# Optimization experiments

Hardware: AMD Instinct MI355X
Metric: run time of the kernel (lower is better)

The kernel has to match this reference:

```python
import jax, jax.numpy as jnp
import numpy as np

N = 50000        # num_nodes
E = 800000       # num_edges
D_IN = 128
D_OUT = 128
BN_EPS = 1e-5    # torch BatchNorm1d default


def setup_inputs() -> dict:
    key = jax.random.key(0)
    ks = jax.random.split(key, 6)
    x = jax.random.normal(ks[0], (N, D_IN), dtype=jnp.float32)
    edge_index = jax.random.randint(ks[1], (2, E), 0, N, dtype=jnp.int64)
    eps = jnp.zeros((1,), dtype=jnp.float32)  # nn.Parameter(torch.tensor([0.0]))
    lim1 = 1.0 / np.sqrt(D_IN)
    lim2 = 1.0 / np.sqrt(D_OUT)
    W1 = jax.random.uniform(ks[2], (D_OUT, D_IN), jnp.float32, -lim1, lim1)
    b1 = jax.random.uniform(ks[3], (D_OUT,), jnp.float32, -lim1, lim1)
    W2 = jax.random.uniform(ks[4], (D_OUT, D_OUT), jnp.float32, -lim2, lim2)
    b2 = jax.random.uniform(ks[5], (D_OUT,), jnp.float32, -lim2, lim2)
    gamma1 = jnp.ones((D_OUT,), jnp.float32)
    beta1 = jnp.zeros((D_OUT,), jnp.float32)
    gamma2 = jnp.ones((D_OUT,), jnp.float32)
    beta2 = jnp.zeros((D_OUT,), jnp.float32)
    return {"x": x, "edge_index": edge_index, "eps": eps,
            "W1": W1, "b1": b1, "gamma1": gamma1, "beta1": beta1,
            "W2": W2, "b2": b2, "gamma2": gamma2, "beta2": beta2}


def _batch_norm(h, gamma, beta):
    # training-mode BatchNorm1d: biased batch variance, eps=1e-5
    mu = h.mean(axis=0)
    var = h.var(axis=0)
    return gamma * (h - mu) * jax.lax.rsqrt(var + BN_EPS) + beta


def reference(x, edge_index, eps, W1, b1, gamma1, beta1, W2, b2, gamma2, beta2):
    row, col = edge_index[0], edge_index[1]
    # agg[v] = sum_{(v,u) in edges} x[u]   (gather + scatter-add)
    agg = jax.ops.segment_sum(x[col], row, num_segments=N)  # [N, D_IN]
    out = (1.0 + eps) * x + agg                              # [N, D_IN]
    h = jax.nn.relu(_batch_norm(out @ W1.T + b1, gamma1, beta1))
    h = jax.nn.relu(_batch_norm(h @ W2.T + b2, gamma2, beta2))
    return h
```

## Files before the change

### kernel.cpp

```cpp
#include <hip/hip_runtime.h>

#define NN 50000
#define EE 800000
#define DD 128
#define BN_EPS 1e-5f
#define XCONV_B 3125
#define BIN_BLOCKS 200
#define BIN_EDGES 4000
#define NBUCK 782
#define BCAP 2048
#define NREP 32
#define GEMM_B 782

typedef __attribute__((ext_vector_type(8))) short bf16x8;
typedef __attribute__((ext_vector_type(4))) float f32x4;
typedef __attribute__((ext_vector_type(8))) unsigned short u16x8;

__device__ inline unsigned short f2bf(float f) {
  unsigned int u = __float_as_uint(f);
  u = (u + 0x7fffu + ((u >> 16) & 1u)) >> 16;
  return (unsigned short)u;
}
__device__ inline float bf2f(unsigned short b) {
  return __uint_as_float(((unsigned int)b) << 16);
}


__global__ __launch_bounds__(256) void k_prep(const float* __restrict__ x,
                                              const float* __restrict__ W1,
                                              const float* __restrict__ W2,
                                              unsigned short* __restrict__ xb,
                                              unsigned short* __restrict__ W1b,
                                              unsigned short* __restrict__ W2b,
                                              int* __restrict__ bcur,
                                              float* __restrict__ reps) {
  const int b = blockIdx.x;
  const int t = threadIdx.x;
  if (b < XCONV_B) {
    const int gid = b * 256 + t;
    const float4 v0 = ((const float4*)x)[gid * 2];
    const float4 v1 = ((const float4*)x)[gid * 2 + 1];
    ushort4 o0, o1;
    o0.x = f2bf(v0.x); o0.y = f2bf(v0.y); o0.z = f2bf(v0.z); o0.w = f2bf(v0.w);
    o1.x = f2bf(v1.x); o1.y = f2bf(v1.y); o1.z = f2bf(v1.z); o1.w = f2bf(v1.w);
    ((ushort4*)xb)[gid * 2] = o0;
    ((ushort4*)xb)[gid * 2 + 1] = o1;
    if (gid < NBUCK) bcur[gid] = 0;
    if (gid < 4 * NREP * DD) reps[gid] = 0.0f;
  } else if (b < XCONV_B + 16) {
    const int gid = (b - XCONV_B) * 256 + t;
    const float4 v = ((const float4*)W1)[gid];
    ushort4 o;
    o.x = f2bf(v.x); o.y = f2bf(v.y); o.z = f2bf(v.z); o.w = f2bf(v.w);
    ((ushort4*)W1b)[gid] = o;
  } else {
    const int gid = (b - XCONV_B - 16) * 256 + t;
    const float4 v = ((const float4*)W2)[gid];
    ushort4 o;
    o.x = f2bf(v.x); o.y = f2bf(v.y); o.z = f2bf(v.z); o.w = f2bf(v.w);
    ((ushort4*)W2b)[gid] = o;
  }
}

__global__ __launch_bounds__(256) void k_bin0(const int* __restrict__ rows,
                                              const int* __restrict__ cols,
                                              int* __restrict__ bcur,
                                              unsigned int* __restrict__ bbuf) {
  __shared__ int hist[NBUCK];
  __shared__ int lbase[NBUCK];
  const int t = threadIdx.x;
  for (int i = t; i < NBUCK; i += 256) hist[i] = 0;
  __syncthreads();
  const int e0 = blockIdx.x * BIN_EDGES;
  int er[16], ec[16];
#pragma unroll
  for (int i = 0; i < 16; ++i) {
    const int idx = t + i * 256;
    if (idx < BIN_EDGES) {
      er[i] = rows[e0 + idx];
      ec[i] = cols[e0 + idx];
      atomicAdd(&hist[er[i] >> 6], 1);
    }
  }
  __syncthreads();
  for (int i = t; i < NBUCK; i += 256) {
    const int c = hist[i];
    lbase[i] = (c > 0) ? atomicAdd(&bcur[i], c) : 0;
    hist[i] = 0;
  }
  __syncthreads();
#pragma unroll
  for (int i = 0; i < 16; ++i) {
    const int idx = t + i * 256;
    if (idx < BIN_EDGES) {
      const int bk = er[i] >> 6;
      const int lp = lbase[bk] + atomicAdd(&hist[bk], 1);
      if (lp < BCAP)
        bbuf[(size_t)bk * BCAP + lp] =
            ((unsigned)(er[i] & 63) << 16) | (unsigned)ec[i];
    }
  }
}

__global__ __launch_bounds__(256) void k_aggb(const unsigned short* __restrict__ xb,
                                              const float* __restrict__ eps,
                                              const int* __restrict__ bcnt,
                                              const unsigned int* __restrict__ bbuf,
                                              unsigned short* __restrict__ h0b) {
  __shared__ unsigned short scols[BCAP];
  __shared__ int rcnt[64];
  __shared__ int roff[65];
  __shared__ int sscan[256];
  const int t = threadIdx.x;
  const int bk = blockIdx.x;
  int n = bcnt[bk];
  n = n < BCAP ? n : BCAP;
  if (t < 64) rcnt[t] = 0;
  __syncthreads();
  unsigned int ent[8];
  int nl = 0;
  for (int i = t; i < n; i += 256) {
    const unsigned int e = bbuf[(size_t)bk * BCAP + i];
    ent[nl++] = e;
    atomicAdd(&rcnt[e >> 16], 1);
  }
  __syncthreads();
  sscan[t] = (t < 64) ? rcnt[t] : 0;
  __syncthreads();
#pragma unroll
  for (int off = 1; off < 64; off <<= 1) {
    const int v = (t >= off) ? sscan[t - off] : 0;
    __syncthreads();
    sscan[t] += v;
    __syncthreads();
  }
  if (t < 64) {
    roff[t] = sscan[t] - rcnt[t];
    rcnt[t] = 0;
  }
  if (t == 63) roff[64] = sscan[63];
  __syncthreads();
  for (int i = 0; i < nl; ++i) {
    const int r = ent[i] >> 16;
    const int pos = roff[r] + atomicAdd(&rcnt[r], 1);
    scols[pos] = (unsigned short)(ent[i] & 0xffffu);
  }
  __syncthreads();
  const int wv = t >> 6;
  const int lane = t & 63;
  const int sub = lane >> 4;
  const int l16 = lane & 15;
  const float s = 1.0f + eps[0];
  for (int r = wv; r < 64; r += 4) {
    const int v = bk * 64 + r;
    if (v >= NN) continue;
    const int beg = roff[r];
    const int end = roff[r + 1];
    float acc[8];
    if (sub == 0) {
      const u16x8 a = *(const u16x8*)(xb + (size_t)v * DD + l16 * 8);
#pragma unroll
      for (int j = 0; j < 8; ++j) acc[j] = s * bf2f(a[j]);
    } else {
#pragma unroll
      for (int j = 0; j < 8; ++j) acc[j] = 0.f;
    }
    int i = beg + sub;
    for (; i + 4 < end; i += 8) {
      const int u0 = scols[i];
      const int u1 = scols[i + 4];
      const u16x8 a = *(const u16x8*)(xb + (size_t)u0 * DD + l16 * 8);
      const u16x8 b = *(const u16x8*)(xb + (size_t)u1 * DD + l16 * 8);
#pragma unroll
      for (int j = 0; j < 8; ++j) acc[j] += bf2f(a[j]) + bf2f(b[j]);
    }
    if (i < end) {
      const int u = scols[i];
      const u16x8 a = *(const u16x8*)(xb + (size_t)u * DD + l16 * 8);
#pragma unroll
      for (int j = 0; j < 8; ++j) acc[j] += bf2f(a[j]);
    }
#pragma unroll
    for (int j = 0; j < 8; ++j) {
      acc[j] += __shfl_xor(acc[j], 16);
      acc[j] += __shfl_xor(acc[j], 32);
    }
    if (sub == 0) {
      u16x8 o;
#pragma unroll
      for (int j = 0; j < 8; ++j) o[j] = f2bf(acc[j]);
      *(u16x8*)(h0b + (size_t)v * DD + l16 * 8) = o;
    }
  }
}

__global__ __launch_bounds__(256) void k_gemm1(const unsigned short* __restrict__ A,
                                               const unsigned short* __restrict__ W,
                                               const float* __restrict__ bias,
                                               unsigned short* __restrict__ outb,
                                               float* __restrict__ sum1r,
                                               float* __restrict__ sumsq1r) {
  __shared__ float bsum[DD];
  __shared__ float bsq[DD];
  const int tid = threadIdx.x;
  const int wv = tid >> 6;
  const int lane = tid & 63;
  const int quad = lane >> 4;
  const int l16 = lane & 15;
  if (tid < DD) { bsum[tid] = 0.f; bsq[tid] = 0.f; }
  __syncthreads();

  const int rowbase = blockIdx.x * 64 + wv * 16 + l16;
  const int arow = rowbase < NN ? rowbase : NN - 1;
  const unsigned short* aptr = A + (size_t)arow * DD + quad * 8;

  f32x4 acc[8];
#pragma unroll
  for (int n = 0; n < 8; ++n) acc[n] = (f32x4){0.f, 0.f, 0.f, 0.f};
#pragma unroll
  for (int kk = 0; kk < 4; ++kk) {
    const bf16x8 af = *(const bf16x8*)(aptr + kk * 32);
#pragma unroll
    for (int n = 0; n < 8; ++n) {
      const bf16x8 bf =
          *(const bf16x8*)(W + (size_t)(n * 16 + l16) * DD + quad * 8 + kk * 32);
      acc[n] = __builtin_amdgcn_mfma_f32_16x16x32_bf16(af, bf, acc[n], 0, 0, 0);
    }
  }
  const int orow0 = blockIdx.x * 64 + wv * 16 + quad * 4;
#pragma unroll
  for (int n = 0; n < 8; ++n) {
    const int col = n * 16 + l16;
    const float bv = bias[col];
    float sv = 0.f, qv = 0.f;
#pragma unroll
    for (int r = 0; r < 4; ++r) {
      const int row = orow0 + r;
      if (row < NN) {
        const float o = acc[n][r] + bv;
        outb[(size_t)row * DD + col] = f2bf(o);
        sv += o; qv += o * o;
      }
    }
    sv += __shfl_xor(sv, 16); qv += __shfl_xor(qv, 16);
    sv += __shfl_xor(sv, 32); qv += __shfl_xor(qv, 32);
    if (quad == 0) { atomicAdd(&bsum[col], sv); atomicAdd(&bsq[col], qv); }
  }
  __syncthreads();
  if (tid < DD) {
    const int rep = (blockIdx.x & (NREP - 1)) * DD;
    atomicAdd(&sum1r[rep + tid], bsum[tid]);
    atomicAdd(&sumsq1r[rep + tid], bsq[tid]);
  }
}

__global__ __launch_bounds__(256) void k_gemm2(const unsigned short* __restrict__ A,
                                               const float* __restrict__ sum1r,
                                               const float* __restrict__ sumsq1r,
                                               const float* __restrict__ gamma,
                                               const float* __restrict__ beta,
                                               const unsigned short* __restrict__ W,
                                               const float* __restrict__ bias,
                                               unsigned short* __restrict__ outb,
                                               float* __restrict__ sum2r,
                                               float* __restrict__ sumsq2r) {
  __shared__ float lsc[DD];
  __shared__ float lsh[DD];
  __shared__ float bsum[DD];
  __shared__ float bsq[DD];
  const int tid = threadIdx.x;
  const int wv = tid >> 6;
  const int lane = tid & 63;
  const int quad = lane >> 4;
  const int l16 = lane & 15;
  if (tid < DD) {
    float sm = 0.f, qm = 0.f;
#pragma unroll
    for (int r = 0; r < NREP; ++r) {
      sm += sum1r[r * DD + tid];
      qm += sumsq1r[r * DD + tid];
    }
    const float inv_n = 1.0f / (float)NN;
    const float mean = sm * inv_n;
    const float var = qm * inv_n - mean * mean;
    const float s = gamma[tid] * rsqrtf(var + BN_EPS);
    lsc[tid] = s;
    lsh[tid] = beta[tid] - mean * s;
    bsum[tid] = 0.f;
    bsq[tid] = 0.f;
  }
  __syncthreads();

  const int rowbase = blockIdx.x * 64 + wv * 16 + l16;
  const int arow = rowbase < NN ? rowbase : NN - 1;
  const unsigned short* aptr = A + (size_t)arow * DD + quad * 8;

  f32x4 acc[8];
#pragma unroll
  for (int n = 0; n < 8; ++n) acc[n] = (f32x4){0.f, 0.f, 0.f, 0.f};
#pragma unroll
  for (int kk = 0; kk < 4; ++kk) {
    const int kbase = kk * 32 + quad * 8;
    const u16x8 a = *(const u16x8*)(aptr + kk * 32);
    const float4 s0 = *(const float4*)&lsc[kbase];
    const float4 s1 = *(const float4*)&lsc[kbase + 4];
    const float4 h0 = *(const float4*)&lsh[kbase];
    const float4 h1 = *(const float4*)&lsh[kbase + 4];
    bf16x8 af;
    af[0] = (short)f2bf(fmaxf(fmaf(s0.x, bf2f(a[0]), h0.x), 0.f));
    af[1] = (short)f2bf(fmaxf(fmaf(s0.y, bf2f(a[1]), h0.y), 0.f));
    af[2] = (short)f2bf(fmaxf(fmaf(s0.z, bf2f(a[2]), h0.z), 0.f));
    af[3] = (short)f2bf(fmaxf(fmaf(s0.w, bf2f(a[3]), h0.w), 0.f));
    af[4] = (short)f2bf(fmaxf(fmaf(s1.x, bf2f(a[4]), h1.x), 0.f));
    af[5] = (short)f2bf(fmaxf(fmaf(s1.y, bf2f(a[5]), h1.y), 0.f));
    af[6] = (short)f2bf(fmaxf(fmaf(s1.z, bf2f(a[6]), h1.z), 0.f));
    af[7] = (short)f2bf(fmaxf(fmaf(s1.w, bf2f(a[7]), h1.w), 0.f));
#pragma unroll
    for (int n = 0; n < 8; ++n) {
      const bf16x8 bf =
          *(const bf16x8*)(W + (size_t)(n * 16 + l16) * DD + kbase);
      acc[n] = __builtin_amdgcn_mfma_f32_16x16x32_bf16(af, bf, acc[n], 0, 0, 0);
    }
  }
  const int orow0 = blockIdx.x * 64 + wv * 16 + quad * 4;
#pragma unroll
  for (int n = 0; n < 8; ++n) {
    const int col = n * 16 + l16;
    const float bv = bias[col];
    float sv = 0.f, qv = 0.f;
#pragma unroll
    for (int r = 0; r < 4; ++r) {
      const int row = orow0 + r;
      if (row < NN) {
        const float o = acc[n][r] + bv;
        outb[(size_t)row * DD + col] = f2bf(o);
        sv += o; qv += o * o;
      }
    }
    sv += __shfl_xor(sv, 16); qv += __shfl_xor(qv, 16);
    sv += __shfl_xor(sv, 32); qv += __shfl_xor(qv, 32);
    if (quad == 0) { atomicAdd(&bsum[col], sv); atomicAdd(&bsq[col], qv); }
  }
  __syncthreads();
  if (tid < DD) {
    const int rep = (blockIdx.x & (NREP - 1)) * DD;
    atomicAdd(&sum2r[rep + tid], bsum[tid]);
    atomicAdd(&sumsq2r[rep + tid], bsq[tid]);
  }
}

__global__ void k_bnstats2(const float* __restrict__ sum2r,
                           const float* __restrict__ sumsq2r,
                           const float* __restrict__ gamma,
                           const float* __restrict__ beta,
                           float* __restrict__ scale,
                           float* __restrict__ shift) {
  const int c = threadIdx.x;
  float sm = 0.f, qm = 0.f;
#pragma unroll
  for (int r = 0; r < NREP; ++r) {
    sm += sum2r[r * DD + c];
    qm += sumsq2r[r * DD + c];
  }
  const float inv_n = 1.0f / (float)NN;
  const float mean = sm * inv_n;
  const float var = qm * inv_n - mean * mean;
  const float sc = gamma[c] * rsqrtf(var + BN_EPS);
  scale[c] = sc;
  shift[c] = beta[c] - mean * sc;
}

__global__ __launch_bounds__(256) void k_bnrelu(const unsigned short* __restrict__ in,
                                                const float* __restrict__ scale,
                                                const float* __restrict__ shift,
                                                float* __restrict__ out) {
  __shared__ float lsc[DD];
  __shared__ float lsh[DD];
  const int t = threadIdx.x;
  if (t < DD) {
    lsc[t] = scale[t];
    lsh[t] = shift[t];
  }
  __syncthreads();
  const int gid = blockIdx.x * 256 + t;
  const int c = (gid & 15) * 8;
  const u16x8 a = ((const u16x8*)in)[gid];
  const float4 sc0 = *(const float4*)&lsc[c];
  const float4 sc1 = *(const float4*)&lsc[c + 4];
  const float4 sh0 = *(const float4*)&lsh[c];
  const float4 sh1 = *(const float4*)&lsh[c + 4];
  float4 o0, o1;
  o0.x = fmaxf(fmaf(sc0.x, bf2f(a[0]), sh0.x), 0.f);
  o0.y = fmaxf(fmaf(sc0.y, bf2f(a[1]), sh0.y), 0.f);
  o0.z = fmaxf(fmaf(sc0.z, bf2f(a[2]), sh0.z), 0.f);
  o0.w = fmaxf(fmaf(sc0.w, bf2f(a[3]), sh0.w), 0.f);
  o1.x = fmaxf(fmaf(sc1.x, bf2f(a[4]), sh1.x), 0.f);
  o1.y = fmaxf(fmaf(sc1.y, bf2f(a[5]), sh1.y), 0.f);
  o1.z = fmaxf(fmaf(sc1.z, bf2f(a[6]), sh1.z), 0.f);
  o1.w = fmaxf(fmaf(sc1.w, bf2f(a[7]), sh1.w), 0.f);
  ((float4*)out)[gid * 2] = o0;
  ((float4*)out)[gid * 2 + 1] = o1;
}

extern "C" void kernel_launch(void* const* d_in, const int* in_sizes, int n_in,
                              void* d_out, int out_size, void* d_ws, size_t ws_size,
                              hipStream_t stream) {
  const float* x = (const float*)d_in[0];
  const int* ei = (const int*)d_in[1];
  const float* eps = (const float*)d_in[2];
  const float* W1 = (const float*)d_in[3];
  const float* b1 = (const float*)d_in[4];
  const float* g1 = (const float*)d_in[5];
  const float* be1 = (const float*)d_in[6];
  const float* W2 = (const float*)d_in[7];
  const float* b2 = (const float*)d_in[8];
  const float* g2 = (const float*)d_in[9];
  const float* be2 = (const float*)d_in[10];
  float* out = (float*)d_out;

  const int* rows = ei;
  const int* cols = ei + EE;

  int* bcur = (int*)d_out;
  unsigned short* xb = (unsigned short*)d_out + 2000000;
  unsigned int* bbuf = (unsigned int*)((char*)d_out + 16800000);
  unsigned short* W1b = (unsigned short*)d_out + 11640000;
  unsigned short* W2b = (unsigned short*)d_out + 11680000;
  float* reps = (float*)d_out + 5875000;
  float* sum1r = reps;
  float* sumsq1r = reps + NREP * DD;
  float* sum2r = reps + 2 * NREP * DD;
  float* sumsq2r = reps + 3 * NREP * DD;

  unsigned short* h0b = (unsigned short*)d_ws;
  unsigned short* h1b = h0b + (size_t)NN * DD;
  unsigned short* h2b = h0b;
  float* stats = (float*)(h0b + (size_t)2 * NN * DD);
  float* scale2 = stats + 0;
  float* shift2 = stats + 128;

  k_prep<<<XCONV_B + 32, 256, 0, stream>>>(x, W1, W2, xb, W1b, W2b, bcur, reps);
  k_bin0<<<BIN_BLOCKS, 256, 0, stream>>>(rows, cols, bcur, bbuf);
  k_aggb<<<NBUCK, 256, 0, stream>>>(xb, eps, bcur, bbuf, h0b);
  k_gemm1<<<GEMM_B, 256, 0, stream>>>(h0b, W1b, b1, h1b, sum1r, sumsq1r);
  k_gemm2<<<GEMM_B, 256, 0, stream>>>(h1b, sum1r, sumsq1r, g1, be1, W2b, b2,
                                      h2b, sum2r, sumsq2r);
  k_bnstats2<<<1, 128, 0, stream>>>(sum2r, sumsq2r, g2, be2, scale2, shift2);
  k_bnrelu<<<(NN * DD / 8) / 256, 256, 0, stream>>>(h2b, scale2, shift2, out);
}
```

Baseline: 214.1 us.

## Fuse neighbor aggregation with first GEMM via shared-memory A tile

Merges the aggregation kernel and the first GEMM into one kernel. Each block's aggregated 64-row bf16 tile is written to padded LDS and fed straight into MFMA, instead of going through a global h0 buffer. This removes one kernel launch and a 12.8MB write plus re-read of the intermediate. In exchange the block uses about 17KB more LDS, which may lower occupancy during the gather-heavy phase.

```diff
diff --git a/kernel.cpp b/kernel.cpp
--- a/kernel.cpp
+++ b/kernel.cpp
@@ -10,7 +10,7 @@
 #define NBUCK 782
 #define BCAP 2048
 #define NREP 32
-#define GEMM_B 782
+#define LDA 136
 
 typedef __attribute__((ext_vector_type(8))) short bf16x8;
 typedef __attribute__((ext_vector_type(4))) float f32x4;
@@ -102,21 +102,32 @@
   }
 }
 
-__global__ __launch_bounds__(256) void k_aggb(const unsigned short* __restrict__ xb,
-                                              const float* __restrict__ eps,
-                                              const int* __restrict__ bcnt,
-                                              const unsigned int* __restrict__ bbuf,
-                                              unsigned short* __restrict__ h0b) {
+__global__ __launch_bounds__(256) void k_aggemm1(
+    const unsigned short* __restrict__ xb, const float* __restrict__ eps,
+    const int* __restrict__ bcnt, const unsigned int* __restrict__ bbuf,
+    const unsigned short* __restrict__ W, const float* __restrict__ bias,
+    unsigned short* __restrict__ outb, float* __restrict__ sum1r,
+    float* __restrict__ sumsq1r) {
   __shared__ unsigned short scols[BCAP];
+  __shared__ unsigned short sA[64 * LDA];
   __shared__ int rcnt[64];
   __shared__ int roff[65];
   __shared__ int sscan[256];
+  __shared__ float bsum[DD];
+  __shared__ float bsq[DD];
   const int t = threadIdx.x;
   const int bk = blockIdx.x;
+  const int wv = t >> 6;
+  const int lane = t & 63;
+  const int sub = lane >> 4;
+  const int l16 = lane & 15;
+
   int n = bcnt[bk];
   n = n < BCAP ? n : BCAP;
   if (t < 64) rcnt[t] = 0;
-  __syncthreads();
+  if (t < DD) { bsum[t] = 0.f; bsq[t] = 0.f; }
+  __syncthreads();
+
   unsigned int ent[8];
   int nl = 0;
   for (int i = t; i < n; i += 256) {
@@ -146,111 +157,91 @@
     scols[pos] = (unsigned short)(ent[i] & 0xffffu);
   }
   __syncthreads();
-  const int wv = t >> 6;
-  const int lane = t & 63;
-  const int sub = lane >> 4;
-  const int l16 = lane & 15;
-  const float s = 1.0f + eps[0];
-  for (int r = wv; r < 64; r += 4) {
-    const int v = bk * 64 + r;
-    if (v >= NN) continue;
-    const int beg = roff[r];
-    const int end = roff[r + 1];
-    float acc[8];
-    if (sub == 0) {
-      const u16x8 a = *(const u16x8*)(xb + (size_t)v * DD + l16 * 8);
-#pragma unroll
-      for (int j = 0; j < 8; ++j) acc[j] = s * bf2f(a[j]);
-    } else {
+
+  {
+    const float s = 1.0f + eps[0];
+    for (int r = wv; r < 64; r += 4) {
+      const int v = bk * 64 + r;
+      float acc[8];
 #pragma unroll
       for (int j = 0; j < 8; ++j) acc[j] = 0.f;
-    }
-    int i = beg + sub;
-    for (; i + 4 < end; i += 8) {
-      const int u0 = scols[i];
-      const int u1 = scols[i + 4];
-      const u16x8 a = *(const u16x8*)(xb + (size_t)u0 * DD + l16 * 8);
-      const u16x8 b = *(const u16x8*)(xb + (size_t)u1 * DD + l16 * 8);
-#pragma unroll
-      for (int j = 0; j < 8; ++j) acc[j] += bf2f(a[j]) + bf2f(b[j]);
-    }
-    if (i < end) {
-      const int u = scols[i];
-      const u16x8 a = *(const u16x8*)(xb + (size_t)u * DD + l16 * 8);
-#pragma unroll
-      for (int j = 0; j < 8; ++j) acc[j] += bf2f(a[j]);
-    }
-#pragma unroll
-    for (int j = 0; j < 8; ++j) {
-      acc[j] += __shfl_xor(acc[j], 16);
-      acc[j] += __shfl_xor(acc[j], 32);
-    }
-    if (sub == 0) {
-      u16x8 o;
-#pragma unroll
-      for (int j = 0; j < 8; ++j) o[j] = f2bf(acc[j]);
-      *(u16x8*)(h0b + (size_t)v * DD + l16 * 8) = o;
-    }
-  }
-}
-
-__global__ __launch_bounds__(256) void k_gemm1(const unsigned short* __restrict__ A,
-                                               const unsigned short* __restrict__ W,
-                                               const float* __restrict__ bias,
-                                               unsigned short* __restrict__ outb,
-                                               float* __restrict__ sum1r,
-                                               float* __restrict__ sumsq1r) {
-  __shared__ float bsum[DD];
-  __shared__ float bsq[DD];
-  const int tid = threadIdx.x;
-  const int wv = tid >> 6;
-  const int lane = tid & 63;
-  const int quad = lane >> 4;
-  const int l16 = lane & 15;
-  if (tid < DD) { bsum[tid] = 0.f; bsq[tid] = 0.f; }
-  __syncthreads();
-
-  const int rowbase = blockIdx.x * 64 + wv * 16 + l16;
-  const int arow = rowbase < NN ? rowbase : NN - 1;
-  const unsigned short* aptr = A + (size_t)arow * DD + quad * 8;
+      if (v < NN) {
+        if (sub == 0) {
+          const u16x8 a = *(const u16x8*)(xb + (size_t)v * DD + l16 * 8);
+#pragma unroll
+          for (int j = 0; j < 8; ++j) acc[j] = s * bf2f(a[j]);
+        }
+        const int beg = roff[r];
+        const int end = roff[r + 1];
+        int i = beg + sub;
+        for (; i + 4 < end; i += 8) {
+          const int u0 = scols[i];
+          const int u1 = scols[i + 4];
+          const u16x8 a = *(const u16x8*)(xb + (size_t)u0 * DD + l16 * 8);
+          const u16x8 b = *(const u16x8*)(xb + (size_t)u1 * DD + l16 * 8);
+#pragma unroll
+          for (int j = 0; j < 8; ++j) acc[j] += bf2f(a[j]) + bf2f(b[j]);
+        }
+        if (i < end) {
+          const int u = scols[i];
+          const u16x8 a = *(const u16x8*)(xb + (size_t)u * DD + l16 * 8);
+#pragma unroll
+          for (int j = 0; j < 8; ++j) acc[j] += bf2f(a[j]);
+        }
+      }
+#pragma unroll
+      for (int j = 0; j < 8; ++j) {
+        acc[j] += __shfl_xor(acc[j], 16);
+        acc[j] += __shfl_xor(acc[j], 32);
+      }
+      if (sub == 0) {
+        u16x8 o;
+#pragma unroll
+        for (int j = 0; j < 8; ++j) o[j] = f2bf(acc[j]);
+        *(u16x8*)(&sA[r * LDA + l16 * 8]) = o;
+      }
+    }
+  }
+  __syncthreads();
 
   f32x4 acc[8];
 #pragma unroll
-  for (int n = 0; n < 8; ++n) acc[n] = (f32x4){0.f, 0.f, 0.f, 0.f};
+  for (int nn = 0; nn < 8; ++nn) acc[nn] = (f32x4){0.f, 0.f, 0.f, 0.f};
 #pragma unroll
   for (int kk = 0; kk < 4; ++kk) {
-    const bf16x8 af = *(const bf16x8*)(aptr + kk * 32);
-#pragma unroll
-    for (int n = 0; n < 8; ++n) {
+    const bf16x8 af =
+        *(const bf16x8*)(&sA[(wv * 16 + l16) * LDA + kk * 32 + sub * 8]);
+#pragma unroll
+    for (int nn = 0; nn < 8; ++nn) {
       const bf16x8 bf =
-          *(const bf16x8*)(W + (size_t)(n * 16 + l16) * DD + quad * 8 + kk * 32);
-      acc[n] = __builtin_amdgcn_mfma_f32_16x16x32_bf16(af, bf, acc[n], 0, 0, 0);
-    }
-  }
-  const int orow0 = blockIdx.x * 64 + wv * 16 + quad * 4;
-#pragma unroll
-  for (int n = 0; n < 8; ++n) {
-    const int col = n * 16 + l16;
+          *(const bf16x8*)(W + (size_t)(nn * 16 + l16) * DD + sub * 8 + kk * 32);
+      acc[nn] = __builtin_amdgcn_mfma_f32_16x16x32_bf16(af, bf, acc[nn], 0, 0, 0);
+    }
+  }
+  const int orow0 = bk * 64 + wv * 16 + sub * 4;
+#pragma unroll
+  for (int nn = 0; nn < 8; ++nn) {
+    const int col = nn * 16 + l16;
     const float bv = bias[col];
     float sv = 0.f, qv = 0.f;
 #pragma unroll
     for (int r = 0; r < 4; ++r) {
       const int row = orow0 + r;
       if (row < NN) {
-        const float o = acc[n][r] + bv;
+        const float o = acc[nn][r] + bv;
         outb[(size_t)row * DD + col] = f2bf(o);
         sv += o; qv += o * o;
       }
     }
     sv += __shfl_xor(sv, 16); qv += __shfl_xor(qv, 16);
     sv += __shfl_xor(sv, 32); qv += __shfl_xor(qv, 32);
-    if (quad == 0) { atomicAdd(&bsum[col], sv); atomicAdd(&bsq[col], qv); }
-  }
-  __syncthreads();
-  if (tid < DD) {
-    const int rep = (blockIdx.x & (NREP - 1)) * DD;
-    atomicAdd(&sum1r[rep + tid], bsum[tid]);
-    atomicAdd(&sumsq1r[rep + tid], bsq[tid]);
+    if (sub == 0) { atomicAdd(&bsum[col], sv); atomicAdd(&bsq[col], qv); }
+  }
+  __syncthreads();
+  if (t < DD) {
+    const int rep = (bk & (NREP - 1)) * DD;
+    atomicAdd(&sum1r[rep + t], bsum[t]);
+    atomicAdd(&sumsq1r[rep + t], bsq[t]);
   }
 }
 
@@ -432,19 +423,18 @@
   float* sum2r = reps + 2 * NREP * DD;
   float* sumsq2r = reps + 3 * NREP * DD;
 
-  unsigned short* h0b = (unsigned short*)d_ws;
-  unsigned short* h1b = h0b + (size_t)NN * DD;
-  unsigned short* h2b = h0b;
-  float* stats = (float*)(h0b + (size_t)2 * NN * DD);
+  unsigned short* h1b = (unsigned short*)d_ws;
+  unsigned short* h2b = h1b + (size_t)NN * DD;
+  float* stats = (float*)(h1b + (size_t)2 * NN * DD);
   float* scale2 = stats + 0;
   float* shift2 = stats + 128;
 
   k_prep<<<XCONV_B + 32, 256, 0, stream>>>(x, W1, W2, xb, W1b, W2b, bcur, reps);
   k_bin0<<<BIN_BLOCKS, 256, 0, stream>>>(rows, cols, bcur, bbuf);
-  k_aggb<<<NBUCK, 256, 0, stream>>>(xb, eps, bcur, bbuf, h0b);
-  k_gemm1<<<GEMM_B, 256, 0, stream>>>(h0b, W1b, b1, h1b, sum1r, sumsq1r);
-  k_gemm2<<<GEMM_B, 256, 0, stream>>>(h1b, sum1r, sumsq1r, g1, be1, W2b, b2,
-                                      h2b, sum2r, sumsq2r);
+  k_aggemm1<<<NBUCK, 256, 0, stream>>>(xb, eps, bcur, bbuf, W1b, b1, h1b,
+                                       sum1r, sumsq1r);
+  k_gemm2<<<NBUCK, 256, 0, stream>>>(h1b, sum1r, sumsq1r, g1, be1, W2b, b2,
+                                     h2b, sum2r, sumsq2r);
   k_bnstats2<<<1, 128, 0, stream>>>(sum2r, sumsq2r, g2, be2, scale2, shift2);
   k_bnrelu<<<(NN * DD / 8) / 256, 256, 0, stream>>>(h2b, scale2, shift2, out);
 }
```

After: 207.8 us. 2.9% less time.
